# Kernel optimization log

Measured on AMD Instinct MI355X. Metric: run time of the kernel, lower is better.

## Reference

```python
import jax, jax.numpy as jnp
import numpy as np

B, P, D, WIDTH, S, HID, ITERS, EPS = 256, 128, 4096, 768, 4, 768, 3, 1e-8
SCALE = WIDTH ** -0.5


def _ln(x, g, b):
    mu = jnp.mean(x, axis=-1, keepdims=True)
    var = jnp.mean((x - mu) ** 2, axis=-1, keepdims=True)
    return (x - mu) / jnp.sqrt(var + 1e-5) * g + b


def setup_inputs() -> dict:
    key = jax.random.key(0)
    ks = jax.random.split(key, 24)
    std = 0.02
    inp = {
        "pixel_values": jax.random.normal(ks[0], (B, P, D), jnp.float32),
        "noise": jax.random.normal(ks[1], (B, S, WIDTH), jnp.float32),
        "W_embed": jax.random.normal(ks[2], (WIDTH, D), jnp.float32) * std,
        "b_embed": jnp.zeros((WIDTH,), jnp.float32),
        "pos_emb": jax.random.normal(ks[3], (P, WIDTH), jnp.float32) * SCALE,
        "slots_mu": jax.random.normal(ks[4], (1, 1, WIDTH), jnp.float32),
        "slots_sigma": jnp.abs(jax.random.normal(ks[5], (1, 1, WIDTH), jnp.float32)),
        "Wq": jax.random.normal(ks[6], (WIDTH, WIDTH), jnp.float32) * std,
        "bq": jnp.zeros((WIDTH,), jnp.float32),
        "Wk": jax.random.normal(ks[7], (WIDTH, WIDTH), jnp.float32) * std,
        "bk": jnp.zeros((WIDTH,), jnp.float32),
        "Wv": jax.random.normal(ks[8], (WIDTH, WIDTH), jnp.float32) * std,
        "bv": jnp.zeros((WIDTH,), jnp.float32),
        "W_ih": jax.random.normal(ks[9], (3 * WIDTH, WIDTH), jnp.float32) * std,
        "W_hh": jax.random.normal(ks[10], (3 * WIDTH, WIDTH), jnp.float32) * std,
        "b_ih": jnp.zeros((3 * WIDTH,), jnp.float32),
        "b_hh": jnp.zeros((3 * WIDTH,), jnp.float32),
        "W1": jax.random.normal(ks[11], (HID, WIDTH), jnp.float32) * std,
        "b1": jnp.zeros((HID,), jnp.float32),
        "W2": jax.random.normal(ks[12], (WIDTH, HID), jnp.float32) * std,
        "b2": jnp.zeros((WIDTH,), jnp.float32),
        "ln_in_g": jnp.ones((WIDTH,), jnp.float32),
        "ln_in_b": jnp.zeros((WIDTH,), jnp.float32),
        "ln_s_g": jnp.ones((WIDTH,), jnp.float32),
        "ln_s_b": jnp.zeros((WIDTH,), jnp.float32),
        "ln_ff_g": jnp.ones((WIDTH,), jnp.float32),
        "ln_ff_b": jnp.zeros((WIDTH,), jnp.float32),
    }
    return inp


def reference(pixel_values, noise, W_embed, b_embed, pos_emb, slots_mu, slots_sigma,
              Wq, bq, Wk, bk, Wv, bv, W_ih, W_hh, b_ih, b_hh,
              W1, b1, W2, b2, ln_in_g, ln_in_b, ln_s_g, ln_s_b, ln_ff_g, ln_ff_b):
    # video embed + positional embedding + layernorm
    inputs = jnp.einsum('bpd,wd->bpw', pixel_values, W_embed) + b_embed + pos_emb
    inputs = _ln(inputs, ln_in_g, ln_in_b)
    k = inputs @ Wk.T + bk  # [B, P, W]
    v = inputs @ Wv.T + bv  # [B, P, W]

    slots = slots_mu + slots_sigma * noise  # [B, S, W]
    for _ in range(ITERS):
        slots_prev = slots
        q = _ln(slots, ln_s_g, ln_s_b) @ Wq.T + bq  # [B, S, W]
        dots = jnp.einsum('bsd,bnd->bsn', q, k) * SCALE  # [B, S, P]
        attn = jax.nn.softmax(dots, axis=1) + EPS  # softmax over slots
        attn = attn / jnp.sum(attn, axis=-1, keepdims=True)
        updates = jnp.einsum('bnd,bsn->bsd', v, attn)  # [B, S, W]
        # GRUCell (PyTorch gate order: r, z, n)
        x = updates.reshape(-1, WIDTH)
        h = slots_prev.reshape(-1, WIDTH)
        gx = x @ W_ih.T + b_ih
        gh = h @ W_hh.T + b_hh
        xr, xz, xn = jnp.split(gx, 3, axis=-1)
        hr, hz, hn = jnp.split(gh, 3, axis=-1)
        r = jax.nn.sigmoid(xr + hr)
        z = jax.nn.sigmoid(xz + hz)
        n = jnp.tanh(xn + r * hn)
        slots = ((1.0 - z) * n + z * h).reshape(B, S, WIDTH)
        # residual MLP
        ff = jax.nn.relu(_ln(slots, ln_ff_g, ln_ff_b) @ W1.T + b1) @ W2.T + b2
        slots = slots + ff
    return slots
```

## Files before the change

### kernel.cpp

```cpp
#include <hip/hip_runtime.h>
#include <hip/hip_bf16.h>
#include <cstdint>
#include <cstddef>

typedef __attribute__((ext_vector_type(8))) short bf16x8;
typedef __attribute__((ext_vector_type(4))) float f32x4;

static __device__ __forceinline__ unsigned short f2bf(float f) {
  uint32_t u = __builtin_bit_cast(uint32_t, f);
  u += 0x7fffu + ((u >> 16) & 1u);
  return (unsigned short)(u >> 16);
}
static __device__ __forceinline__ float bf2f(unsigned short h) {
  return __builtin_bit_cast(float, (uint32_t)h << 16);
}
static __device__ __forceinline__ float ldf(const float* p, size_t i) { return p[i]; }
static __device__ __forceinline__ float ldf(const unsigned short* p, size_t i) { return bf2f(p[i]); }

template <bool A_F32>
__global__ __launch_bounds__(256) void gemm_bt(
    const void* __restrict__ Ap, const unsigned short* __restrict__ Bt,
    const float* __restrict__ bias, const float* __restrict__ pos,
    const float* __restrict__ res, float* __restrict__ outf,
    unsigned short* __restrict__ outb, int M, int N, int K, int relu) {
  __shared__ alignas(16) unsigned short Al[128][40];
  __shared__ alignas(16) unsigned short Bl[128][40];
  const int tid = threadIdx.x;
  const int lane = tid & 63;
  const int wid = tid >> 6;
  const int wr = wid >> 1;
  const int wc = wid & 1;
  const int bm = blockIdx.y * 128;
  const int bn = blockIdx.x * 128;

  f32x4 acc[4][4];
#pragma unroll
  for (int m = 0; m < 4; ++m)
#pragma unroll
    for (int n = 0; n < 4; ++n) acc[m][n] = (f32x4){0.f, 0.f, 0.f, 0.f};

  const int srow = tid >> 2;
  const int sc8 = (tid & 3) << 3;

  for (int kk = 0; kk < K; kk += 32) {
    __syncthreads();
#pragma unroll
    for (int j = 0; j < 2; ++j) {
      const int row = j * 64 + srow;
      if constexpr (A_F32) {
        const float* s = (const float*)Ap + (size_t)(bm + row) * K + kk + sc8;
        const float4 f0 = *(const float4*)s;
        const float4 f1 = *(const float4*)(s + 4);
        bf16x8 h;
        h[0] = (short)f2bf(f0.x); h[1] = (short)f2bf(f0.y);
        h[2] = (short)f2bf(f0.z); h[3] = (short)f2bf(f0.w);
        h[4] = (short)f2bf(f1.x); h[5] = (short)f2bf(f1.y);
        h[6] = (short)f2bf(f1.z); h[7] = (short)f2bf(f1.w);
        *(bf16x8*)&Al[row][sc8] = h;
      } else {
        *(bf16x8*)&Al[row][sc8] =
            *(const bf16x8*)((const unsigned short*)Ap + (size_t)(bm + row) * K + kk + sc8);
      }
      *(bf16x8*)&Bl[row][sc8] = *(const bf16x8*)(Bt + (size_t)(bn + row) * K + kk + sc8);
    }
    __syncthreads();
    bf16x8 av[4], bw[4];
#pragma unroll
    for (int m = 0; m < 4; ++m)
      av[m] = *(const bf16x8*)&Al[wr * 64 + m * 16 + (lane & 15)][(lane >> 4) * 8];
#pragma unroll
    for (int n = 0; n < 4; ++n)
      bw[n] = *(const bf16x8*)&Bl[wc * 64 + n * 16 + (lane & 15)][(lane >> 4) * 8];
#pragma unroll
    for (int m = 0; m < 4; ++m)
#pragma unroll
      for (int n = 0; n < 4; ++n)
        acc[m][n] = __builtin_amdgcn_mfma_f32_16x16x32_bf16(av[m], bw[n], acc[m][n], 0, 0, 0);
  }

#pragma unroll
  for (int m = 0; m < 4; ++m) {
#pragma unroll
    for (int n = 0; n < 4; ++n) {
      const int col = bn + wc * 64 + n * 16 + (lane & 15);
#pragma unroll
      for (int r = 0; r < 4; ++r) {
        const int row = bm + wr * 64 + m * 16 + (lane >> 4) * 4 + r;
        float v = acc[m][n][r] + bias[col];
        if (pos) v += pos[(size_t)(row & 127) * 768 + col];
        if (relu) v = v > 0.f ? v : 0.f;
        if (res) v += res[(size_t)row * N + col];
        if (outf) outf[(size_t)row * N + col] = v;
        if (outb) outb[(size_t)row * N + col] = f2bf(v);
      }
    }
  }
}

template <typename T>
__global__ __launch_bounds__(256) void ln768(const T* __restrict__ in,
                                             const float* __restrict__ g,
                                             const float* __restrict__ be,
                                             unsigned short* __restrict__ out) {
  const int tid = threadIdx.x;
  const size_t base = (size_t)blockIdx.x * 768;
  const float x0 = ldf(in, base + tid);
  const float x1 = ldf(in, base + tid + 256);
  const float x2 = ldf(in, base + tid + 512);
  float s = x0 + x1 + x2;
  float sq = x0 * x0 + x1 * x1 + x2 * x2;
  for (int off = 32; off; off >>= 1) {
    s += __shfl_xor(s, off);
    sq += __shfl_xor(sq, off);
  }
  __shared__ float red[2][4];
  const int lane = tid & 63, wid = tid >> 6;
  if (lane == 0) { red[0][wid] = s; red[1][wid] = sq; }
  __syncthreads();
  s = red[0][0] + red[0][1] + red[0][2] + red[0][3];
  sq = red[1][0] + red[1][1] + red[1][2] + red[1][3];
  const float mu = s * (1.f / 768.f);
  const float var = sq * (1.f / 768.f) - mu * mu;
  const float rstd = rsqrtf(var + 1e-5f);
  out[base + tid]       = f2bf((x0 - mu) * rstd * g[tid] + be[tid]);
  out[base + tid + 256] = f2bf((x1 - mu) * rstd * g[tid + 256] + be[tid + 256]);
  out[base + tid + 512] = f2bf((x2 - mu) * rstd * g[tid + 512] + be[tid + 512]);
}

__global__ __launch_bounds__(256) void slot_attn(
    const float* __restrict__ q, const unsigned short* __restrict__ k,
    const unsigned short* __restrict__ v, unsigned short* __restrict__ xout) {
  const int b = blockIdx.x;
  const int tid = threadIdx.x;
  const int lane = tid & 63, wv = tid >> 6;
  __shared__ float qs[3072];
  __shared__ float wn[4][128];
  __shared__ float ssum[4];
  for (int i = tid; i < 3072; i += 256) qs[i] = q[(size_t)b * 3072 + i];
  if (tid < 4) ssum[tid] = 0.f;
  __syncthreads();
  const float scale = 0.03608439182435161f;
  for (int n = wv; n < 128; n += 4) {
    const unsigned short* kp = k + ((size_t)b * 128 + n) * 768;
    float p0 = 0.f, p1 = 0.f, p2 = 0.f, p3 = 0.f;
    for (int j = 0; j < 12; ++j) {
      const int d = j * 64 + lane;
      const float kv = bf2f(kp[d]);
      p0 += qs[d] * kv;
      p1 += qs[768 + d] * kv;
      p2 += qs[1536 + d] * kv;
      p3 += qs[2304 + d] * kv;
    }
    for (int off = 32; off; off >>= 1) {
      p0 += __shfl_xor(p0, off);
      p1 += __shfl_xor(p1, off);
      p2 += __shfl_xor(p2, off);
      p3 += __shfl_xor(p3, off);
    }
    if (lane == 0) {
      const float d0 = p0 * scale, d1 = p1 * scale, d2 = p2 * scale, d3 = p3 * scale;
      const float mx = fmaxf(fmaxf(d0, d1), fmaxf(d2, d3));
      const float e0 = expf(d0 - mx), e1 = expf(d1 - mx), e2 = expf(d2 - mx), e3 = expf(d3 - mx);
      const float inv = 1.f / (e0 + e1 + e2 + e3);
      const float w0 = e0 * inv + 1e-8f, w1 = e1 * inv + 1e-8f;
      const float w2 = e2 * inv + 1e-8f, w3 = e3 * inv + 1e-8f;
      wn[0][n] = w0; wn[1][n] = w1; wn[2][n] = w2; wn[3][n] = w3;
      atomicAdd(&ssum[0], w0); atomicAdd(&ssum[1], w1);
      atomicAdd(&ssum[2], w2); atomicAdd(&ssum[3], w3);
    }
  }
  __syncthreads();
  const float i0 = 1.f / ssum[0], i1 = 1.f / ssum[1];
  const float i2 = 1.f / ssum[2], i3 = 1.f / ssum[3];
  float acc[4][3] = {};
  const unsigned short* vb = v + (size_t)b * 128 * 768;
  for (int n = 0; n < 128; ++n) {
    const float w0 = wn[0][n], w1 = wn[1][n], w2 = wn[2][n], w3 = wn[3][n];
#pragma unroll
    for (int c = 0; c < 3; ++c) {
      const float vv = bf2f(vb[(size_t)n * 768 + tid + c * 256]);
      acc[0][c] += w0 * vv; acc[1][c] += w1 * vv;
      acc[2][c] += w2 * vv; acc[3][c] += w3 * vv;
    }
  }
  const float is[4] = {i0, i1, i2, i3};
#pragma unroll
  for (int s = 0; s < 4; ++s)
#pragma unroll
    for (int c = 0; c < 3; ++c)
      xout[((size_t)b * 4 + s) * 768 + tid + c * 256] = f2bf(acc[s][c] * is[s]);
}

__global__ __launch_bounds__(256) void gru_gate(const float* __restrict__ gx,
                                                const float* __restrict__ gh,
                                                float* __restrict__ S) {
  const int i = blockIdx.y;
  const int j = blockIdx.x * 256 + threadIdx.x;
  const size_t g0 = (size_t)i * 2304 + j;
  const float xr = gx[g0], xz = gx[g0 + 768], xn = gx[g0 + 1536];
  const float hr = gh[g0], hz = gh[g0 + 768], hn = gh[g0 + 1536];
  const size_t si = (size_t)i * 768 + j;
  const float h = S[si];
  const float r = 1.f / (1.f + expf(-(xr + hr)));
  const float z = 1.f / (1.f + expf(-(xz + hz)));
  const float nn = tanhf(xn + r * hn);
  S[si] = (1.f - z) * nn + z * h;
}

__global__ __launch_bounds__(256) void init_slots(const float* __restrict__ noise,
                                                  const float* __restrict__ mu,
                                                  const float* __restrict__ sg,
                                                  float* __restrict__ S) {
  const int i = blockIdx.y;
  const int j = blockIdx.x * 256 + threadIdx.x;
  const size_t idx = (size_t)i * 768 + j;
  S[idx] = mu[j] + sg[j] * noise[idx];
}

__global__ __launch_bounds__(256) void cvt_bf(const float* __restrict__ in,
                                              unsigned short* __restrict__ out, int n) {
  const int i = blockIdx.x * 256 + threadIdx.x;
  if (i < n) out[i] = f2bf(in[i]);
}

extern "C" void kernel_launch(void* const* d_in, const int* in_sizes, int n_in,
                              void* d_out, int out_size, void* d_ws, size_t ws_size,
                              hipStream_t stream) {
  const float* pixel   = (const float*)d_in[0];
  const float* noise   = (const float*)d_in[1];
  const float* W_embed = (const float*)d_in[2];
  const float* b_embed = (const float*)d_in[3];
  const float* pos_emb = (const float*)d_in[4];
  const float* s_mu    = (const float*)d_in[5];
  const float* s_sg    = (const float*)d_in[6];
  const float* Wq  = (const float*)d_in[7];  const float* bq  = (const float*)d_in[8];
  const float* Wk  = (const float*)d_in[9];  const float* bk  = (const float*)d_in[10];
  const float* Wv  = (const float*)d_in[11]; const float* bvp = (const float*)d_in[12];
  const float* Wih = (const float*)d_in[13]; const float* Whh = (const float*)d_in[14];
  const float* bih = (const float*)d_in[15]; const float* bhh = (const float*)d_in[16];
  const float* W1  = (const float*)d_in[17]; const float* b1  = (const float*)d_in[18];
  const float* W2  = (const float*)d_in[19]; const float* b2  = (const float*)d_in[20];
  const float* ling = (const float*)d_in[21]; const float* linb = (const float*)d_in[22];
  const float* lsg  = (const float*)d_in[23]; const float* lsb  = (const float*)d_in[24];
  const float* lfg  = (const float*)d_in[25]; const float* lfb  = (const float*)d_in[26];

  char* wsp = (char*)d_ws;
  auto alloc = [&](size_t bytes) -> void* {
    void* p = (void*)wsp;
    wsp += (bytes + 255) & ~(size_t)255;
    return p;
  };
  unsigned short* Wemb_b = (unsigned short*)alloc(768ull * 4096 * 2);
  unsigned short* Wq_b   = (unsigned short*)alloc(768ull * 768 * 2);
  unsigned short* Wk_b   = (unsigned short*)alloc(768ull * 768 * 2);
  unsigned short* Wv_b   = (unsigned short*)alloc(768ull * 768 * 2);
  unsigned short* Wih_b  = (unsigned short*)alloc(2304ull * 768 * 2);
  unsigned short* Whh_b  = (unsigned short*)alloc(2304ull * 768 * 2);
  unsigned short* W1_b   = (unsigned short*)alloc(768ull * 768 * 2);
  unsigned short* W2_b   = (unsigned short*)alloc(768ull * 768 * 2);
  unsigned short* inpre  = (unsigned short*)alloc(32768ull * 768 * 2);
  unsigned short* inpn   = (unsigned short*)alloc(32768ull * 768 * 2);
  unsigned short* kb     = (unsigned short*)alloc(32768ull * 768 * 2);
  unsigned short* vb     = (unsigned short*)alloc(32768ull * 768 * 2);
  float* S   = (float*)alloc(1024ull * 768 * 4);
  float* qf  = (float*)alloc(1024ull * 768 * 4);
  float* gxf = (float*)alloc(1024ull * 2304 * 4);
  float* ghf = (float*)alloc(1024ull * 2304 * 4);
  unsigned short* hb   = (unsigned short*)alloc(1024ull * 768 * 2);
  unsigned short* lnsb = (unsigned short*)alloc(1024ull * 768 * 2);
  unsigned short* xb   = (unsigned short*)alloc(1024ull * 768 * 2);
  unsigned short* lnfb = (unsigned short*)alloc(1024ull * 768 * 2);
  unsigned short* m1b  = (unsigned short*)alloc(1024ull * 768 * 2);

  auto cvt = [&](const float* src, unsigned short* dst, int n) {
    cvt_bf<<<dim3((n + 255) / 256), dim3(256), 0, stream>>>(src, dst, n);
  };
  cvt(W_embed, Wemb_b, 768 * 4096);
  cvt(Wq, Wq_b, 768 * 768);
  cvt(Wk, Wk_b, 768 * 768);
  cvt(Wv, Wv_b, 768 * 768);
  cvt(Wih, Wih_b, 2304 * 768);
  cvt(Whh, Whh_b, 2304 * 768);
  cvt(W1, W1_b, 768 * 768);
  cvt(W2, W2_b, 768 * 768);

  gemm_bt<true><<<dim3(6, 256), dim3(256), 0, stream>>>(
      pixel, Wemb_b, b_embed, pos_emb, nullptr, nullptr, inpre, 32768, 768, 4096, 0);
  ln768<unsigned short><<<dim3(32768), dim3(256), 0, stream>>>(inpre, ling, linb, inpn);
  gemm_bt<false><<<dim3(6, 256), dim3(256), 0, stream>>>(
      inpn, Wk_b, bk, nullptr, nullptr, nullptr, kb, 32768, 768, 768, 0);
  gemm_bt<false><<<dim3(6, 256), dim3(256), 0, stream>>>(
      inpn, Wv_b, bvp, nullptr, nullptr, nullptr, vb, 32768, 768, 768, 0);
  init_slots<<<dim3(3, 1024), dim3(256), 0, stream>>>(noise, s_mu, s_sg, S);

  for (int it = 0; it < 3; ++it) {
    cvt(S, hb, 1024 * 768);
    ln768<float><<<dim3(1024), dim3(256), 0, stream>>>(S, lsg, lsb, lnsb);
    gemm_bt<false><<<dim3(6, 8), dim3(256), 0, stream>>>(
        lnsb, Wq_b, bq, nullptr, nullptr, qf, nullptr, 1024, 768, 768, 0);
    slot_attn<<<dim3(256), dim3(256), 0, stream>>>(qf, kb, vb, xb);
    gemm_bt<false><<<dim3(18, 8), dim3(256), 0, stream>>>(
        xb, Wih_b, bih, nullptr, nullptr, gxf, nullptr, 1024, 2304, 768, 0);
    gemm_bt<false><<<dim3(18, 8), dim3(256), 0, stream>>>(
        hb, Whh_b, bhh, nullptr, nullptr, ghf, nullptr, 1024, 2304, 768, 0);
    gru_gate<<<dim3(3, 1024), dim3(256), 0, stream>>>(gxf, ghf, S);
    ln768<float><<<dim3(1024), dim3(256), 0, stream>>>(S, lfg, lfb, lnfb);
    gemm_bt<false><<<dim3(6, 8), dim3(256), 0, stream>>>(
        lnfb, W1_b, b1, nullptr, nullptr, nullptr, m1b, 1024, 768, 768, 1);
    float* outp = (it == 2) ? (float*)d_out : S;
    gemm_bt<false><<<dim3(6, 8), dim3(256), 0, stream>>>(
        m1b, W2_b, b2, nullptr, S, outp, nullptr, 1024, 768, 768, 0);
  }
}
```

Measured before the change: 1.952 ms.

## Overhaul GEMM loading, fuse K/V projection, GRU+LN, and batch weight conversions

Rewrites the GEMM to use direct global-to-LDS loads, packed bf16 conversion, templated wider tiles (BN=256, 8 waves) and workgroup swizzling for the large GEMMs. K and V projections are merged into one GEMM over a concatenated weight, and the two GRU gate GEMMs are launched as one grid. The GRU gate is fused with the following layernorm, the bf16 copy of slots is written inside the W2 epilogue, and the weight conversions collapse into one launch. The slot attention kernel is restructured for vectorized loads over the interleaved K/V buffer. The unpadded LDS layout may introduce bank conflicts.

Result: faster. 1.665 ms (-14.7%).

```diff
diff --git a/kernel.cpp b/kernel.cpp
--- a/kernel.cpp
+++ b/kernel.cpp
@@ -14,54 +14,80 @@
 static __device__ __forceinline__ float bf2f(unsigned short h) {
   return __builtin_bit_cast(float, (uint32_t)h << 16);
 }
-static __device__ __forceinline__ float ldf(const float* p, size_t i) { return p[i]; }
-static __device__ __forceinline__ float ldf(const unsigned short* p, size_t i) { return bf2f(p[i]); }
-
-template <bool A_F32>
-__global__ __launch_bounds__(256) void gemm_bt(
+static __device__ __forceinline__ void gload16(const void* g, void* l) {
+  __builtin_amdgcn_global_load_lds(
+      (const __attribute__((address_space(1))) unsigned int*)g,
+      (__attribute__((address_space(3))) unsigned int*)l, 16, 0, 0);
+}
+
+template <bool A_F32, bool SWZ, int BN, int NW>
+__global__ __launch_bounds__(NW * 64) void gemm_bt(
     const void* __restrict__ Ap, const unsigned short* __restrict__ Bt,
     const float* __restrict__ bias, const float* __restrict__ pos,
     const float* __restrict__ res, float* __restrict__ outf,
-    unsigned short* __restrict__ outb, int M, int N, int K, int relu) {
-  __shared__ alignas(16) unsigned short Al[128][40];
-  __shared__ alignas(16) unsigned short Bl[128][40];
+    unsigned short* __restrict__ outb, int M, int N, int K, int relu,
+    const void* __restrict__ Ap2, const unsigned short* __restrict__ Bt2,
+    const float* __restrict__ bias2, float* __restrict__ outf2) {
+  constexpr int T = NW * 64;
+  constexpr int WC = NW / 2;
+  __shared__ alignas(16) unsigned short Al[128][A_F32 ? 40 : 32];
+  __shared__ alignas(16) unsigned short Bl[BN][32];
+  if (blockIdx.z) { Ap = Ap2; Bt = Bt2; bias = bias2; outf = outf2; }
   const int tid = threadIdx.x;
-  const int lane = tid & 63;
-  const int wid = tid >> 6;
-  const int wr = wid >> 1;
-  const int wc = wid & 1;
-  const int bm = blockIdx.y * 128;
-  const int bn = blockIdx.x * 128;
+  const int lane = tid & 63, wid = tid >> 6;
+  const int wr = wid / WC, wc = wid % WC;
+  int bx = blockIdx.x, by = blockIdx.y;
+  if constexpr (SWZ) {
+    const int gx = gridDim.x;
+    const int nwg = gx * gridDim.y;
+    const int flat = by * gx + bx;
+    const int cpx = nwg >> 3;
+    const int logical = (flat & 7) * cpx + (flat >> 3);
+    by = logical / gx;
+    bx = logical % gx;
+  }
+  const int bm = by * 128, bn = bx * BN;
 
   f32x4 acc[4][4];
 #pragma unroll
   for (int m = 0; m < 4; ++m)
 #pragma unroll
     for (int n = 0; n < 4; ++n) acc[m][n] = (f32x4){0.f, 0.f, 0.f, 0.f};
-
-  const int srow = tid >> 2;
-  const int sc8 = (tid & 3) << 3;
 
   for (int kk = 0; kk < K; kk += 32) {
     __syncthreads();
-#pragma unroll
-    for (int j = 0; j < 2; ++j) {
-      const int row = j * 64 + srow;
-      if constexpr (A_F32) {
+    if constexpr (A_F32) {
+      const int sc8 = (tid & 3) << 3;
+#pragma unroll
+      for (int j = 0; j < 4096 / (T * 8); ++j) {
+        const int row = j * (T / 4) + (tid >> 2);
         const float* s = (const float*)Ap + (size_t)(bm + row) * K + kk + sc8;
         const float4 f0 = *(const float4*)s;
         const float4 f1 = *(const float4*)(s + 4);
-        bf16x8 h;
-        h[0] = (short)f2bf(f0.x); h[1] = (short)f2bf(f0.y);
-        h[2] = (short)f2bf(f0.z); h[3] = (short)f2bf(f0.w);
-        h[4] = (short)f2bf(f1.x); h[5] = (short)f2bf(f1.y);
-        h[6] = (short)f2bf(f1.z); h[7] = (short)f2bf(f1.w);
-        *(bf16x8*)&Al[row][sc8] = h;
-      } else {
-        *(bf16x8*)&Al[row][sc8] =
-            *(const bf16x8*)((const unsigned short*)Ap + (size_t)(bm + row) * K + kk + sc8);
+        unsigned int r0, r1, r2, r3;
+        asm("v_cvt_pk_bf16_f32 %0, %1, %2" : "=v"(r0) : "v"(f0.x), "v"(f0.y));
+        asm("v_cvt_pk_bf16_f32 %0, %1, %2" : "=v"(r1) : "v"(f0.z), "v"(f0.w));
+        asm("v_cvt_pk_bf16_f32 %0, %1, %2" : "=v"(r2) : "v"(f1.x), "v"(f1.y));
+        asm("v_cvt_pk_bf16_f32 %0, %1, %2" : "=v"(r3) : "v"(f1.z), "v"(f1.w));
+        uint4 pk; pk.x = r0; pk.y = r1; pk.z = r2; pk.w = r3;
+        *(uint4*)&Al[row][sc8] = pk;
       }
-      *(bf16x8*)&Bl[row][sc8] = *(const bf16x8*)(Bt + (size_t)(bn + row) * K + kk + sc8);
+    } else {
+#pragma unroll
+      for (int j = 0; j < 512 / T; ++j) {
+        const int chunk = j * T + tid;
+        const int row = chunk >> 2, c8 = (chunk & 3) << 3;
+        const unsigned short* src =
+            (const unsigned short*)Ap + (size_t)(bm + row) * K + kk + c8;
+        gload16(src, (char*)&Al[0][0] + (size_t)((j * T + (tid & ~63)) << 4));
+      }
+    }
+#pragma unroll
+    for (int j = 0; j < (BN * 4) / T; ++j) {
+      const int chunk = j * T + tid;
+      const int row = chunk >> 2, c8 = (chunk & 3) << 3;
+      const unsigned short* src = Bt + (size_t)(bn + row) * K + kk + c8;
+      gload16(src, (char*)&Bl[0][0] + (size_t)((j * T + (tid & ~63)) << 4));
     }
     __syncthreads();
     bf16x8 av[4], bw[4];
@@ -83,10 +109,11 @@
 #pragma unroll
     for (int n = 0; n < 4; ++n) {
       const int col = bn + wc * 64 + n * 16 + (lane & 15);
+      const float bc = bias[col];
 #pragma unroll
       for (int r = 0; r < 4; ++r) {
         const int row = bm + wr * 64 + m * 16 + (lane >> 4) * 4 + r;
-        float v = acc[m][n][r] + bias[col];
+        float v = acc[m][n][r] + bc;
         if (pos) v += pos[(size_t)(row & 127) * 768 + col];
         if (relu) v = v > 0.f ? v : 0.f;
         if (res) v += res[(size_t)row * N + col];
@@ -97,18 +124,25 @@
   }
 }
 
-template <typename T>
-__global__ __launch_bounds__(256) void ln768(const T* __restrict__ in,
+template <bool F32IN>
+__global__ __launch_bounds__(256) void ln768(const void* __restrict__ in,
                                              const float* __restrict__ g,
                                              const float* __restrict__ be,
                                              unsigned short* __restrict__ out) {
   const int tid = threadIdx.x;
   const size_t base = (size_t)blockIdx.x * 768;
-  const float x0 = ldf(in, base + tid);
-  const float x1 = ldf(in, base + tid + 256);
-  const float x2 = ldf(in, base + tid + 512);
-  float s = x0 + x1 + x2;
-  float sq = x0 * x0 + x1 * x1 + x2 * x2;
+  float x[4] = {0.f, 0.f, 0.f, 0.f};
+  if (tid < 192) {
+    if constexpr (F32IN) {
+      const float4 f = *(const float4*)((const float*)in + base + tid * 4);
+      x[0] = f.x; x[1] = f.y; x[2] = f.z; x[3] = f.w;
+    } else {
+      const ushort4 u = *(const ushort4*)((const unsigned short*)in + base + tid * 4);
+      x[0] = bf2f(u.x); x[1] = bf2f(u.y); x[2] = bf2f(u.z); x[3] = bf2f(u.w);
+    }
+  }
+  float s = x[0] + x[1] + x[2] + x[3];
+  float sq = x[0] * x[0] + x[1] * x[1] + x[2] * x[2] + x[3] * x[3];
   for (int off = 32; off; off >>= 1) {
     s += __shfl_xor(s, off);
     sq += __shfl_xor(sq, off);
@@ -122,105 +156,211 @@
   const float mu = s * (1.f / 768.f);
   const float var = sq * (1.f / 768.f) - mu * mu;
   const float rstd = rsqrtf(var + 1e-5f);
-  out[base + tid]       = f2bf((x0 - mu) * rstd * g[tid] + be[tid]);
-  out[base + tid + 256] = f2bf((x1 - mu) * rstd * g[tid + 256] + be[tid + 256]);
-  out[base + tid + 512] = f2bf((x2 - mu) * rstd * g[tid + 512] + be[tid + 512]);
+  if (tid < 192) {
+    ushort4 o;
+    o.x = f2bf((x[0] - mu) * rstd * g[tid * 4 + 0] + be[tid * 4 + 0]);
+    o.y = f2bf((x[1] - mu) * rstd * g[tid * 4 + 1] + be[tid * 4 + 1]);
+    o.z = f2bf((x[2] - mu) * rstd * g[tid * 4 + 2] + be[tid * 4 + 2]);
+    o.w = f2bf((x[3] - mu) * rstd * g[tid * 4 + 3] + be[tid * 4 + 3]);
+    *(ushort4*)(out + base + tid * 4) = o;
+  }
 }
 
 __global__ __launch_bounds__(256) void slot_attn(
-    const float* __restrict__ q, const unsigned short* __restrict__ k,
-    const unsigned short* __restrict__ v, unsigned short* __restrict__ xout) {
+    const float* __restrict__ q, const unsigned short* __restrict__ kv,
+    unsigned short* __restrict__ xout) {
   const int b = blockIdx.x;
   const int tid = threadIdx.x;
-  const int lane = tid & 63, wv = tid >> 6;
-  __shared__ float qs[3072];
+  const int lane = tid & 63, w = tid >> 6;
+  __shared__ float qs[4][768];
   __shared__ float wn[4][128];
-  __shared__ float ssum[4];
-  for (int i = tid; i < 3072; i += 256) qs[i] = q[(size_t)b * 3072 + i];
-  if (tid < 4) ssum[tid] = 0.f;
-  __syncthreads();
-  const float scale = 0.03608439182435161f;
-  for (int n = wv; n < 128; n += 4) {
-    const unsigned short* kp = k + ((size_t)b * 128 + n) * 768;
-    float p0 = 0.f, p1 = 0.f, p2 = 0.f, p3 = 0.f;
-    for (int j = 0; j < 12; ++j) {
-      const int d = j * 64 + lane;
-      const float kv = bf2f(kp[d]);
-      p0 += qs[d] * kv;
-      p1 += qs[768 + d] * kv;
-      p2 += qs[1536 + d] * kv;
-      p3 += qs[2304 + d] * kv;
-    }
-    for (int off = 32; off; off >>= 1) {
-      p0 += __shfl_xor(p0, off);
-      p1 += __shfl_xor(p1, off);
-      p2 += __shfl_xor(p2, off);
-      p3 += __shfl_xor(p3, off);
-    }
+  __shared__ float red2[96][4][8];
+  __shared__ float csw[2][4];
+  const float* qb = q + (size_t)b * 3072;
+  for (int i = tid; i < 768; i += 256)
+    ((float4*)&qs[0][0])[i] = ((const float4*)qb)[i];
+  __syncthreads();
+
+  float qreg[4][8], qreg2[4][8];
+#pragma unroll
+  for (int s = 0; s < 4; ++s) {
+    *(float4*)&qreg[s][0] = *(const float4*)&qs[s][lane * 8];
+    *(float4*)&qreg[s][4] = *(const float4*)&qs[s][lane * 8 + 4];
+  }
+  if (lane < 32) {
+#pragma unroll
+    for (int s = 0; s < 4; ++s) {
+      *(float4*)&qreg2[s][0] = *(const float4*)&qs[s][512 + lane * 8];
+      *(float4*)&qreg2[s][4] = *(const float4*)&qs[s][512 + lane * 8 + 4];
+    }
+  }
+
+  const unsigned short* kbase = kv + (size_t)b * 128 * 1536;
+  for (int n = w; n < 128; n += 4) {
+    const unsigned short* kp = kbase + (size_t)n * 1536;
+    const bf16x8 k0 = *(const bf16x8*)&kp[lane * 8];
+    float p[4] = {0.f, 0.f, 0.f, 0.f};
+#pragma unroll
+    for (int e = 0; e < 8; ++e) {
+      const float kx = bf2f((unsigned short)k0[e]);
+      p[0] += qreg[0][e] * kx; p[1] += qreg[1][e] * kx;
+      p[2] += qreg[2][e] * kx; p[3] += qreg[3][e] * kx;
+    }
+    if (lane < 32) {
+      const bf16x8 k1 = *(const bf16x8*)&kp[512 + lane * 8];
+#pragma unroll
+      for (int e = 0; e < 8; ++e) {
+        const float kx = bf2f((unsigned short)k1[e]);
+        p[0] += qreg2[0][e] * kx; p[1] += qreg2[1][e] * kx;
+        p[2] += qreg2[2][e] * kx; p[3] += qreg2[3][e] * kx;
+      }
+    }
+#pragma unroll
+    for (int s = 0; s < 4; ++s)
+      for (int off = 32; off; off >>= 1) p[s] += __shfl_xor(p[s], off);
     if (lane == 0) {
-      const float d0 = p0 * scale, d1 = p1 * scale, d2 = p2 * scale, d3 = p3 * scale;
-      const float mx = fmaxf(fmaxf(d0, d1), fmaxf(d2, d3));
-      const float e0 = expf(d0 - mx), e1 = expf(d1 - mx), e2 = expf(d2 - mx), e3 = expf(d3 - mx);
-      const float inv = 1.f / (e0 + e1 + e2 + e3);
-      const float w0 = e0 * inv + 1e-8f, w1 = e1 * inv + 1e-8f;
-      const float w2 = e2 * inv + 1e-8f, w3 = e3 * inv + 1e-8f;
-      wn[0][n] = w0; wn[1][n] = w1; wn[2][n] = w2; wn[3][n] = w3;
-      atomicAdd(&ssum[0], w0); atomicAdd(&ssum[1], w1);
-      atomicAdd(&ssum[2], w2); atomicAdd(&ssum[3], w3);
-    }
-  }
-  __syncthreads();
-  const float i0 = 1.f / ssum[0], i1 = 1.f / ssum[1];
-  const float i2 = 1.f / ssum[2], i3 = 1.f / ssum[3];
-  float acc[4][3] = {};
-  const unsigned short* vb = v + (size_t)b * 128 * 768;
-  for (int n = 0; n < 128; ++n) {
-    const float w0 = wn[0][n], w1 = wn[1][n], w2 = wn[2][n], w3 = wn[3][n];
-#pragma unroll
-    for (int c = 0; c < 3; ++c) {
-      const float vv = bf2f(vb[(size_t)n * 768 + tid + c * 256]);
-      acc[0][c] += w0 * vv; acc[1][c] += w1 * vv;
-      acc[2][c] += w2 * vv; acc[3][c] += w3 * vv;
-    }
-  }
-  const float is[4] = {i0, i1, i2, i3};
+      wn[0][n] = p[0]; wn[1][n] = p[1]; wn[2][n] = p[2]; wn[3][n] = p[3];
+    }
+  }
+  __syncthreads();
+
+  float myw[4] = {0.f, 0.f, 0.f, 0.f};
+  if (tid < 128) {
+    const float scale = 0.03608439182435161f;
+    const float d0 = wn[0][tid] * scale, d1 = wn[1][tid] * scale;
+    const float d2 = wn[2][tid] * scale, d3 = wn[3][tid] * scale;
+    const float mx = fmaxf(fmaxf(d0, d1), fmaxf(d2, d3));
+    const float e0 = expf(d0 - mx), e1 = expf(d1 - mx);
+    const float e2 = expf(d2 - mx), e3 = expf(d3 - mx);
+    const float inv = 1.f / (e0 + e1 + e2 + e3);
+    myw[0] = e0 * inv + 1e-8f; myw[1] = e1 * inv + 1e-8f;
+    myw[2] = e2 * inv + 1e-8f; myw[3] = e3 * inv + 1e-8f;
+    wn[0][tid] = myw[0]; wn[1][tid] = myw[1];
+    wn[2][tid] = myw[2]; wn[3][tid] = myw[3];
+  }
+  float cs[4] = {myw[0], myw[1], myw[2], myw[3]};
 #pragma unroll
   for (int s = 0; s < 4; ++s)
-#pragma unroll
-    for (int c = 0; c < 3; ++c)
-      xout[((size_t)b * 4 + s) * 768 + tid + c * 256] = f2bf(acc[s][c] * is[s]);
-}
-
-__global__ __launch_bounds__(256) void gru_gate(const float* __restrict__ gx,
-                                                const float* __restrict__ gh,
-                                                float* __restrict__ S) {
-  const int i = blockIdx.y;
-  const int j = blockIdx.x * 256 + threadIdx.x;
-  const size_t g0 = (size_t)i * 2304 + j;
-  const float xr = gx[g0], xz = gx[g0 + 768], xn = gx[g0 + 1536];
-  const float hr = gh[g0], hz = gh[g0 + 768], hn = gh[g0 + 1536];
-  const size_t si = (size_t)i * 768 + j;
-  const float h = S[si];
-  const float r = 1.f / (1.f + expf(-(xr + hr)));
-  const float z = 1.f / (1.f + expf(-(xz + hz)));
-  const float nn = tanhf(xn + r * hn);
-  S[si] = (1.f - z) * nn + z * h;
+    for (int off = 32; off; off >>= 1) cs[s] += __shfl_xor(cs[s], off);
+  if (tid < 128 && lane == 0) {
+    csw[w][0] = cs[0]; csw[w][1] = cs[1]; csw[w][2] = cs[2]; csw[w][3] = cs[3];
+  }
+  __syncthreads();
+  const float inv_s[4] = {1.f / (csw[0][0] + csw[1][0]), 1.f / (csw[0][1] + csw[1][1]),
+                          1.f / (csw[0][2] + csw[1][2]), 1.f / (csw[0][3] + csw[1][3])};
+
+  float acc[4][8] = {};
+  const int c = tid % 96, h = tid / 96;
+  if (tid < 192) {
+    const unsigned short* vbase = kbase + 768 + (size_t)h * 64 * 1536 + c * 8;
+#pragma unroll 4
+    for (int n = 0; n < 64; ++n) {
+      const bf16x8 vv = *(const bf16x8*)(vbase + (size_t)n * 1536);
+      const int nn = h * 64 + n;
+      const float w0 = wn[0][nn], w1 = wn[1][nn], w2 = wn[2][nn], w3 = wn[3][nn];
+#pragma unroll
+      for (int e = 0; e < 8; ++e) {
+        const float f = bf2f((unsigned short)vv[e]);
+        acc[0][e] += w0 * f; acc[1][e] += w1 * f;
+        acc[2][e] += w2 * f; acc[3][e] += w3 * f;
+      }
+    }
+  }
+  if (tid >= 96 && tid < 192) {
+#pragma unroll
+    for (int s = 0; s < 4; ++s)
+#pragma unroll
+      for (int e = 0; e < 8; ++e) red2[c][s][e] = acc[s][e];
+  }
+  __syncthreads();
+  if (tid < 96) {
+#pragma unroll
+    for (int s = 0; s < 4; ++s) {
+      bf16x8 o;
+#pragma unroll
+      for (int e = 0; e < 8; ++e)
+        o[e] = (short)f2bf((acc[s][e] + red2[c][s][e]) * inv_s[s]);
+      *(bf16x8*)&xout[((size_t)b * 4 + s) * 768 + c * 8] = o;
+    }
+  }
+}
+
+__global__ __launch_bounds__(256) void gru_ln(
+    const float* __restrict__ gx, const float* __restrict__ gh,
+    float* __restrict__ S, const float* __restrict__ g,
+    const float* __restrict__ be, unsigned short* __restrict__ out) {
+  const int i = blockIdx.x;
+  const int tid = threadIdx.x;
+  float sn[3];
+#pragma unroll
+  for (int cc = 0; cc < 3; ++cc) {
+    const int j = tid + cc * 256;
+    const size_t g0 = (size_t)i * 2304 + j;
+    const float xr = gx[g0], xz = gx[g0 + 768], xn = gx[g0 + 1536];
+    const float hr = gh[g0], hz = gh[g0 + 768], hn = gh[g0 + 1536];
+    const float h = S[(size_t)i * 768 + j];
+    const float r = 1.f / (1.f + expf(-(xr + hr)));
+    const float z = 1.f / (1.f + expf(-(xz + hz)));
+    const float nn = tanhf(xn + r * hn);
+    sn[cc] = (1.f - z) * nn + z * h;
+    S[(size_t)i * 768 + j] = sn[cc];
+  }
+  float s = sn[0] + sn[1] + sn[2];
+  float sq = sn[0] * sn[0] + sn[1] * sn[1] + sn[2] * sn[2];
+  for (int off = 32; off; off >>= 1) {
+    s += __shfl_xor(s, off);
+    sq += __shfl_xor(sq, off);
+  }
+  __shared__ float red[2][4];
+  const int lane = tid & 63, wid = tid >> 6;
+  if (lane == 0) { red[0][wid] = s; red[1][wid] = sq; }
+  __syncthreads();
+  s = red[0][0] + red[0][1] + red[0][2] + red[0][3];
+  sq = red[1][0] + red[1][1] + red[1][2] + red[1][3];
+  const float mu = s * (1.f / 768.f);
+  const float var = sq * (1.f / 768.f) - mu * mu;
+  const float rstd = rsqrtf(var + 1e-5f);
+#pragma unroll
+  for (int cc = 0; cc < 3; ++cc) {
+    const int j = tid + cc * 256;
+    out[(size_t)i * 768 + j] = f2bf((sn[cc] - mu) * rstd * g[j] + be[j]);
+  }
 }
 
 __global__ __launch_bounds__(256) void init_slots(const float* __restrict__ noise,
                                                   const float* __restrict__ mu,
                                                   const float* __restrict__ sg,
-                                                  float* __restrict__ S) {
+                                                  float* __restrict__ S,
+                                                  unsigned short* __restrict__ hb) {
   const int i = blockIdx.y;
   const int j = blockIdx.x * 256 + threadIdx.x;
   const size_t idx = (size_t)i * 768 + j;
-  S[idx] = mu[j] + sg[j] * noise[idx];
-}
-
-__global__ __launch_bounds__(256) void cvt_bf(const float* __restrict__ in,
-                                              unsigned short* __restrict__ out, int n) {
-  const int i = blockIdx.x * 256 + threadIdx.x;
-  if (i < n) out[i] = f2bf(in[i]);
+  const float v = mu[j] + sg[j] * noise[idx];
+  S[idx] = v;
+  hb[idx] = f2bf(v);
+}
+
+struct CvtJobs {
+  const float* src[8];
+  unsigned short* dst[8];
+  int n[8];
+};
+__global__ __launch_bounds__(256) void cvt_all(CvtJobs jb) {
+  const int seg = blockIdx.y;
+  const int i = (blockIdx.x * 256 + threadIdx.x) * 4;
+  if (i < jb.n[seg]) {
+    const float4 f = *(const float4*)&jb.src[seg][i];
+    ushort4 o;
+    o.x = f2bf(f.x); o.y = f2bf(f.y); o.z = f2bf(f.z); o.w = f2bf(f.w);
+    *(ushort4*)&jb.dst[seg][i] = o;
+  }
+}
+
+__global__ __launch_bounds__(256) void concat_bias(const float* __restrict__ a,
+                                                   const float* __restrict__ b,
+                                                   float* __restrict__ o) {
+  const int j = blockIdx.x * 256 + threadIdx.x;
+  o[j] = j < 768 ? a[j] : b[j - 768];
 }
 
 extern "C" void kernel_launch(void* const* d_in, const int* in_sizes, int n_in,
@@ -252,16 +392,15 @@
   };
   unsigned short* Wemb_b = (unsigned short*)alloc(768ull * 4096 * 2);
   unsigned short* Wq_b   = (unsigned short*)alloc(768ull * 768 * 2);
-  unsigned short* Wk_b   = (unsigned short*)alloc(768ull * 768 * 2);
-  unsigned short* Wv_b   = (unsigned short*)alloc(768ull * 768 * 2);
+  unsigned short* kvW    = (unsigned short*)alloc(1536ull * 768 * 2);
   unsigned short* Wih_b  = (unsigned short*)alloc(2304ull * 768 * 2);
   unsigned short* Whh_b  = (unsigned short*)alloc(2304ull * 768 * 2);
   unsigned short* W1_b   = (unsigned short*)alloc(768ull * 768 * 2);
   unsigned short* W2_b   = (unsigned short*)alloc(768ull * 768 * 2);
+  float* bkv             = (float*)alloc(1536ull * 4);
   unsigned short* inpre  = (unsigned short*)alloc(32768ull * 768 * 2);
   unsigned short* inpn   = (unsigned short*)alloc(32768ull * 768 * 2);
-  unsigned short* kb     = (unsigned short*)alloc(32768ull * 768 * 2);
-  unsigned short* vb     = (unsigned short*)alloc(32768ull * 768 * 2);
+  unsigned short* kvb    = (unsigned short*)alloc(32768ull * 1536 * 2);
   float* S   = (float*)alloc(1024ull * 768 * 4);
   float* qf  = (float*)alloc(1024ull * 768 * 4);
   float* gxf = (float*)alloc(1024ull * 2304 * 4);
@@ -272,43 +411,43 @@
   unsigned short* lnfb = (unsigned short*)alloc(1024ull * 768 * 2);
   unsigned short* m1b  = (unsigned short*)alloc(1024ull * 768 * 2);
 
-  auto cvt = [&](const float* src, unsigned short* dst, int n) {
-    cvt_bf<<<dim3((n + 255) / 256), dim3(256), 0, stream>>>(src, dst, n);
-  };
-  cvt(W_embed, Wemb_b, 768 * 4096);
-  cvt(Wq, Wq_b, 768 * 768);
-  cvt(Wk, Wk_b, 768 * 768);
-  cvt(Wv, Wv_b, 768 * 768);
-  cvt(Wih, Wih_b, 2304 * 768);
-  cvt(Whh, Whh_b, 2304 * 768);
-  cvt(W1, W1_b, 768 * 768);
-  cvt(W2, W2_b, 768 * 768);
-
-  gemm_bt<true><<<dim3(6, 256), dim3(256), 0, stream>>>(
-      pixel, Wemb_b, b_embed, pos_emb, nullptr, nullptr, inpre, 32768, 768, 4096, 0);
-  ln768<unsigned short><<<dim3(32768), dim3(256), 0, stream>>>(inpre, ling, linb, inpn);
-  gemm_bt<false><<<dim3(6, 256), dim3(256), 0, stream>>>(
-      inpn, Wk_b, bk, nullptr, nullptr, nullptr, kb, 32768, 768, 768, 0);
-  gemm_bt<false><<<dim3(6, 256), dim3(256), 0, stream>>>(
-      inpn, Wv_b, bvp, nullptr, nullptr, nullptr, vb, 32768, 768, 768, 0);
-  init_slots<<<dim3(3, 1024), dim3(256), 0, stream>>>(noise, s_mu, s_sg, S);
+  CvtJobs jb;
+  jb.src[0] = W_embed; jb.dst[0] = Wemb_b;            jb.n[0] = 768 * 4096;
+  jb.src[1] = Wq;      jb.dst[1] = Wq_b;              jb.n[1] = 768 * 768;
+  jb.src[2] = Wk;      jb.dst[2] = kvW;               jb.n[2] = 768 * 768;
+  jb.src[3] = Wv;      jb.dst[3] = kvW + 768 * 768;   jb.n[3] = 768 * 768;
+  jb.src[4] = Wih;     jb.dst[4] = Wih_b;             jb.n[4] = 2304 * 768;
+  jb.src[5] = Whh;     jb.dst[5] = Whh_b;             jb.n[5] = 2304 * 768;
+  jb.src[6] = W1;      jb.dst[6] = W1_b;              jb.n[6] = 768 * 768;
+  jb.src[7] = W2;      jb.dst[7] = W2_b;              jb.n[7] = 768 * 768;
+  cvt_all<<<dim3(3072, 8), dim3(256), 0, stream>>>(jb);
+  concat_bias<<<dim3(6), dim3(256), 0, stream>>>(bk, bvp, bkv);
+
+  gemm_bt<true, true, 256, 8><<<dim3(3, 256), dim3(512), 0, stream>>>(
+      pixel, Wemb_b, b_embed, pos_emb, nullptr, nullptr, inpre, 32768, 768, 4096, 0,
+      nullptr, nullptr, nullptr, nullptr);
+  ln768<false><<<dim3(32768), dim3(256), 0, stream>>>(inpre, ling, linb, inpn);
+  gemm_bt<false, true, 256, 8><<<dim3(6, 256), dim3(512), 0, stream>>>(
+      inpn, kvW, bkv, nullptr, nullptr, nullptr, kvb, 32768, 1536, 768, 0,
+      nullptr, nullptr, nullptr, nullptr);
+  init_slots<<<dim3(3, 1024), dim3(256), 0, stream>>>(noise, s_mu, s_sg, S, hb);
 
   for (int it = 0; it < 3; ++it) {
-    cvt(S, hb, 1024 * 768);
-    ln768<float><<<dim3(1024), dim3(256), 0, stream>>>(S, lsg, lsb, lnsb);
-    gemm_bt<false><<<dim3(6, 8), dim3(256), 0, stream>>>(
-        lnsb, Wq_b, bq, nullptr, nullptr, qf, nullptr, 1024, 768, 768, 0);
-    slot_attn<<<dim3(256), dim3(256), 0, stream>>>(qf, kb, vb, xb);
-    gemm_bt<false><<<dim3(18, 8), dim3(256), 0, stream>>>(
-        xb, Wih_b, bih, nullptr, nullptr, gxf, nullptr, 1024, 2304, 768, 0);
-    gemm_bt<false><<<dim3(18, 8), dim3(256), 0, stream>>>(
-        hb, Whh_b, bhh, nullptr, nullptr, ghf, nullptr, 1024, 2304, 768, 0);
-    gru_gate<<<dim3(3, 1024), dim3(256), 0, stream>>>(gxf, ghf, S);
-    ln768<float><<<dim3(1024), dim3(256), 0, stream>>>(S, lfg, lfb, lnfb);
-    gemm_bt<false><<<dim3(6, 8), dim3(256), 0, stream>>>(
-        lnfb, W1_b, b1, nullptr, nullptr, nullptr, m1b, 1024, 768, 768, 1);
+    ln768<true><<<dim3(1024), dim3(256), 0, stream>>>(S, lsg, lsb, lnsb);
+    gemm_bt<false, false, 128, 4><<<dim3(6, 8), dim3(256), 0, stream>>>(
+        lnsb, Wq_b, bq, nullptr, nullptr, qf, nullptr, 1024, 768, 768, 0,
+        nullptr, nullptr, nullptr, nullptr);
+    slot_attn<<<dim3(256), dim3(256), 0, stream>>>(qf, kvb, xb);
+    gemm_bt<false, false, 128, 4><<<dim3(18, 8, 2), dim3(256), 0, stream>>>(
+        xb, Wih_b, bih, nullptr, nullptr, gxf, nullptr, 1024, 2304, 768, 0,
+        hb, Whh_b, bhh, ghf);
+    gru_ln<<<dim3(1024), dim3(256), 0, stream>>>(gxf, ghf, S, lfg, lfb, lnfb);
+    gemm_bt<false, false, 128, 4><<<dim3(6, 8), dim3(256), 0, stream>>>(
+        lnfb, W1_b, b1, nullptr, nullptr, nullptr, m1b, 1024, 768, 768, 1,
+        nullptr, nullptr, nullptr, nullptr);
     float* outp = (it == 2) ? (float*)d_out : S;
-    gemm_bt<false><<<dim3(6, 8), dim3(256), 0, stream>>>(
-        m1b, W2_b, b2, nullptr, S, outp, nullptr, 1024, 768, 768, 0);
-  }
-}
+    gemm_bt<false, false, 128, 4><<<dim3(6, 8), dim3(256), 0, stream>>>(
+        m1b, W2_b, b2, nullptr, S, outp, hb, 1024, 768, 768, 0,
+        nullptr, nullptr, nullptr, nullptr);
+  }
+}
```
